# Kernel optimization log

Hardware: AMD Instinct MI355X
Metric: run time of the kernel (lower is better)

## Reference

```python
import jax, jax.numpy as jnp
import numpy as np

N_NODES = 20000
NUM_STEPS = 6
SIGNS = (1.0, -1.0, 1.0, -1.0, 1.0, -1.0)  # TF_POS, TF_NEG, PPI_POS, PPI_NEG, UNDIR, MIRNA_NEG


def setup_inputs() -> dict:
    key = jax.random.key(0)
    ks = jax.random.split(key, 12)
    B, N, E, H, C = 64, N_NODES, 400000, 64, 32
    return {
        "ctl_base": jax.random.normal(ks[0], (B, N), jnp.float32),
        "u_raw": jax.random.normal(ks[1], (B, N), jnp.float32),
        "cell_idx": jax.random.randint(ks[2], (B,), 0, C, jnp.int32),
        "edge_src": jax.random.randint(ks[3], (6, E), 0, N, jnp.int32),
        "edge_dst": jax.random.randint(ks[4], (6, E), 0, N, jnp.int32),
        "edge_val": jax.random.uniform(ks[5], (6, E), jnp.float32),
        "g_logits": jnp.zeros((6,), jnp.float32),
        "alpha_logits": jnp.zeros((NUM_STEPS,), jnp.float32),
        "cell_emb": jax.random.normal(ks[6], (C, H), jnp.float32),
        "W1": jax.random.normal(ks[7], (3, H), jnp.float32) * 0.1,
        "b1": jnp.zeros((H,), jnp.float32),
        "W2": jax.random.normal(ks[8], (H, 1), jnp.float32) * 0.1,
        "b2": jnp.zeros((1,), jnp.float32),
    }


def _spmm_right(h, src, dst, val):
    # out[b, j] = sum_{e: dst[e]==j} h[b, src[e]] * val[e]   (== h @ A)
    gathered = h.T[src] * val[:, None]  # [E, B]
    return jax.ops.segment_sum(gathered, dst, num_segments=N_NODES).T  # [B, N]


def reference(ctl_base, u_raw, g_logits, alpha_logits, cell_emb,
              W1, b1, W2, b2, edge_val, edge_src, edge_dst, cell_idx):
    g = jax.nn.softplus(g_logits)          # [6] relation gates
    alphas = jax.nn.sigmoid(alpha_logits)  # [num_steps]
    h0 = u_raw
    h = u_raw
    for k in range(NUM_STEPS):
        msg = jnp.zeros_like(h)
        for r in range(6):
            msg = msg + SIGNS[r] * g[r] * _spmm_right(h, edge_src[r], edge_dst[r], edge_val[r])
        a = alphas[k]
        h = a * h0 + (1.0 - a) * msg
    # decode: stack [ctl, u_raw, hK] -> [B, N, 3]
    x = jnp.stack([ctl_base, u_raw, h], axis=-1)
    hd = jax.nn.relu(jnp.einsum('bnf,fh->bnh', x, W1) + b1)  # [B, N, H]
    hd = hd + cell_emb[cell_idx][:, None, :]
    y = (jnp.einsum('bnh,ho->bno', hd, W2) + b2)[..., 0]  # [B, N]
    return y
```

## Files before the change

kernel.cpp:

```cpp
#include <hip/hip_runtime.h>

#define N_NODES 20000
#define HID 64
#define NSTEPS 6
#define NSLICE 8
#define SLICE_SZ (N_NODES / NSLICE)
#define SUBB 64
#define NBLK (NSLICE * SUBB)
#define TBLK ((N_NODES + 63) / 64)
#define NB1 512
#define CBLK ((N_NODES + 255) / 256)
#define MAGIC 13422

typedef _Float16 h8_t __attribute__((ext_vector_type(8)));
typedef unsigned u4_t __attribute__((ext_vector_type(4)));

union U16H { unsigned short u; _Float16 h; };
union U4H8 { uint4 u; _Float16 h[8]; };

__device__ __forceinline__ _Float16 us_as_h(unsigned short s) { U16H u; u.u = s; return u.h; }
__device__ __forceinline__ unsigned short h_as_us(_Float16 h) { U16H u; u.h = h; return u.u; }

__device__ __forceinline__ int slice_of(int d) {
    return (int)(((unsigned)d * (unsigned)MAGIC) >> 25);
}
__device__ __forceinline__ float softplusf_(float x) {
    return (x > 0.f) ? (x + log1pf(expf(-x))) : log1pf(expf(x));
}
__device__ __forceinline__ float sigmoidf_(float x) {
    return 1.f / (1.f + expf(-x));
}

__global__ __launch_bounds__(256) void count8_kernel(const int* __restrict__ edst,
                                                     int* __restrict__ gcnt, int TE,
                                                     u4_t* __restrict__ egq, long long egq_n) {
    u4_t z = {0u, 0u, 0u, 0u};
    for (long long i = (long long)blockIdx.x * 256 + threadIdx.x; i < egq_n;
         i += (long long)NB1 * 256)
        __builtin_nontemporal_store(z, egq + i);

    __shared__ int lh[8];
    int bk = blockIdx.x;
    int lane = threadIdx.x & 63;
    if (threadIdx.x < 8) lh[threadIdx.x] = 0;
    __syncthreads();
    int chunk = ((TE + NB1 - 1) / NB1 + 255) & ~255;
    int lo = bk * chunk;
    int hi = min(lo + chunk, TE);
    int my = 0;
    for (int ii = 0; ii < chunk; ii += 256) {
        int i = lo + ii + (int)threadIdx.x;
        bool act = i < hi;
        int s = -1;
        if (act) s = slice_of(__builtin_nontemporal_load(edst + i));
#pragma unroll
        for (int q = 0; q < 8; ++q) {
            unsigned long long b = __ballot(s == q);
            if (lane == q) my += (int)__popcll(b);
        }
    }
    if (lane < 8) atomicAdd(&lh[lane], my);
    __syncthreads();
    if (threadIdx.x < 8) gcnt[bk * 8 + threadIdx.x] = lh[threadIdx.x];
}

__global__ __launch_bounds__(256) void scan8_kernel(const int* __restrict__ gcnt,
                                                    int* __restrict__ blkoff,
                                                    int* __restrict__ bbase,
                                                    const float* __restrict__ g_logits,
                                                    const float* __restrict__ alpha_logits,
                                                    const int* __restrict__ cell_idx,
                                                    const float* __restrict__ cell_emb,
                                                    const float* __restrict__ W2,
                                                    const float* __restrict__ b2,
                                                    float* __restrict__ gsign,
                                                    float* __restrict__ alph,
                                                    float* __restrict__ cell_dot) {
    __shared__ int psum[8][33];
    int tid = threadIdx.x;
    int s = tid >> 5, g = tid & 31;
    const int per = NB1 / 32;
    int sum = 0;
    for (int b = g * per; b < (g + 1) * per; ++b) sum += gcnt[b * 8 + s];
    psum[s][g] = sum;
    __syncthreads();
    if (tid < 8) {
        int run = 0;
        for (int i = 0; i < 32; ++i) { int v = psum[tid][i]; psum[tid][i] = run; run += v; }
        psum[tid][32] = run;
    }
    __syncthreads();
    int run = psum[s][g];
    for (int b = g * per; b < (g + 1) * per; ++b) {
        blkoff[b * 8 + s] = run;
        run += gcnt[b * 8 + s];
    }
    if (tid == 0) {
        int acc = 0;
        bbase[0] = 0;
        for (int q = 0; q < 8; ++q) { acc += psum[q][32]; bbase[q + 1] = acc; }
    }
    if (tid < 64) {
        if (tid < 6) gsign[tid] = ((tid & 1) ? -1.f : 1.f) * softplusf_(g_logits[tid]);
        if (tid < NSTEPS) alph[tid] = sigmoidf_(alpha_logits[tid]);
        int ci = cell_idx[tid];
        float acc = b2[0];
        for (int hh = 0; hh < HID; ++hh) acc = fmaf(cell_emb[ci * HID + hh], W2[hh], acc);
        cell_dot[tid] = acc;
    }
}

__global__ __launch_bounds__(256) void bucket_kernel(const int* __restrict__ esrc,
                                                     const int* __restrict__ edst,
                                                     const float* __restrict__ eval,
                                                     const float* __restrict__ gsign,
                                                     const int* __restrict__ blkoff,
                                                     const int* __restrict__ bbase,
                                                     int2* __restrict__ bucket,
                                                     int E, int TE) {
    __shared__ int lcur[8];
    int bk = blockIdx.x;
    int lane = threadIdx.x & 63;
    if (threadIdx.x < 8) lcur[threadIdx.x] = bbase[threadIdx.x] + blkoff[bk * 8 + threadIdx.x];
    __syncthreads();
    int chunk = ((TE + NB1 - 1) / NB1 + 255) & ~255;
    int lo = bk * chunk;
    int hi = min(lo + chunk, TE);
    for (int ii = 0; ii < chunk; ii += 256) {
        int i = lo + ii + (int)threadIdx.x;
        bool act = i < hi;
        int s = -1, meta = 0, cb = 0;
        if (act) {
            int d  = __builtin_nontemporal_load(edst + i);
            int sv = __builtin_nontemporal_load(esrc + i);
            float ev = __builtin_nontemporal_load(eval + i);
            s = slice_of(d);
            int dl = d - s * SLICE_SZ;
            meta = sv | (dl << 16);
            int r = (i >= E) + (i >= 2 * E) + (i >= 3 * E) + (i >= 4 * E) + (i >= 5 * E);
            cb = __float_as_int(gsign[r] * ev);
        }
        int pos = 0;
#pragma unroll
        for (int q = 0; q < 8; ++q) {
            unsigned long long b = __ballot(s == q);
            if (b) {
                int leader = (int)__ffsll(b) - 1;
                int base = 0;
                if (lane == leader) base = atomicAdd(&lcur[q], (int)__popcll(b));
                base = __shfl(base, leader);
                if (s == q) pos = base + (int)__popcll(b & ((1ull << lane) - 1ull));
            }
        }
        if (act) bucket[pos] = make_int2(meta, cb);
    }
}

__global__ __launch_bounds__(256) void hist2db_kernel(const int2* __restrict__ bucket,
                                                      const int* __restrict__ bbase,
                                                      int* __restrict__ blkcnt) {
    __shared__ int lh[SLICE_SZ];
    int bk = blockIdx.x;
    int slice = bk & (NSLICE - 1);
    int sub = bk >> 3;
    for (int b = threadIdx.x; b < SLICE_SZ; b += 256) lh[b] = 0;
    __syncthreads();
    int lo = bbase[slice];
    int total = bbase[slice + 1] - lo;
    int chunk = ((total + SUBB - 1) / SUBB + 255) & ~255;
    int beg = lo + sub * chunk;
    int end = min(beg + chunk, lo + total);
    const int* mp = (const int*)bucket;
    for (int i = beg + (int)threadIdx.x; i < end; i += 256) {
        int meta = __builtin_nontemporal_load(mp + 2 * (size_t)i);
        atomicAdd(&lh[((unsigned)meta) >> 16], 1);
    }
    __syncthreads();
    int* out = blkcnt + (size_t)(slice * SUBB + sub) * SLICE_SZ;
    for (int b = threadIdx.x; b < SLICE_SZ; b += 256) out[b] = lh[b];
}

__global__ __launch_bounds__(256) void colscan_kernel(int* __restrict__ blkcnt,
                                                      int* __restrict__ counts,
                                                      int* __restrict__ blksum) {
    int n = blockIdx.x * 256 + threadIdx.x;
    int run = 0;
    if (n < N_NODES) {
        int slice = n / SLICE_SZ, bin = n % SLICE_SZ;
        size_t base = (size_t)slice * SUBB * SLICE_SZ + bin;
#pragma unroll 8
        for (int s = 0; s < SUBB; ++s) {
            size_t idx = base + (size_t)s * SLICE_SZ;
            int t = blkcnt[idx];
            blkcnt[idx] = run;
            run += t;
        }
        counts[n] = run;
    }
    int g = (n < N_NODES) ? ((run + 7) >> 3) : 0;
#pragma unroll
    for (int st = 1; st < 64; st <<= 1) g += __shfl_xor(g, st, 64);
    __shared__ int wsum[4];
    if ((threadIdx.x & 63) == 0) wsum[threadIdx.x >> 6] = g;
    __syncthreads();
    if (threadIdx.x == 0) blksum[blockIdx.x] = wsum[0] + wsum[1] + wsum[2] + wsum[3];
}

__global__ __launch_bounds__(256) void scan2_kernel(const int* __restrict__ counts,
                                                    const int* __restrict__ blksum,
                                                    int* __restrict__ grp_ptr, int n) {
    int b = blockIdx.x;
    int tid = threadIdx.x, lane = tid & 63, wid = tid >> 6;
    int i = b * 256 + tid;
    int v = (i < n) ? ((counts[i] + 7) >> 3) : 0;
    int x = v;
#pragma unroll
    for (int st = 1; st < 64; st <<= 1) {
        int t = __shfl_up(x, st, 64);
        if (lane >= st) x += t;
    }
    __shared__ int wsum[4];
    if (lane == 63) wsum[wid] = x;
    int s = ((lane < b) ? blksum[lane] : 0) +
            ((lane + 64 < b) ? blksum[lane + 64] : 0);
#pragma unroll
    for (int st = 1; st < 64; st <<= 1) s += __shfl_xor(s, st, 64);
    __syncthreads();
    int woff = s;
    if (wid > 0) woff += wsum[0];
    if (wid > 1) woff += wsum[1];
    if (wid > 2) woff += wsum[2];
    int off = woff + x - v;
    if (i < n) grp_ptr[i] = off;
    if (i == n - 1) grp_ptr[n] = off + v;
}

__global__ __launch_bounds__(256) void scatter2b_kernel(const int2* __restrict__ bucket,
                                                        const int* __restrict__ bbase,
                                                        const int* __restrict__ grp_ptr,
                                                        const int* __restrict__ blkcnt,
                                                        unsigned* __restrict__ eg,
                                                        const float* __restrict__ u_raw,
                                                        float* __restrict__ u_t,
                                                        _Float16* __restrict__ uh) {
    __shared__ float smem[64 * 65];
    int bk = blockIdx.x;
    if (bk >= NBLK) {
        float(*tile)[65] = (float(*)[65])smem;
        int c0 = (bk - NBLK) * 64;
        int tx = threadIdx.x & 63, ty = threadIdx.x >> 6;
#pragma unroll
        for (int i = 0; i < 16; ++i) {
            int c = c0 + tx;
            tile[ty + i * 4][tx] = (c < N_NODES) ? u_raw[(size_t)(ty + i * 4) * N_NODES + c] : 0.f;
        }
        __syncthreads();
#pragma unroll
        for (int i = 0; i < 16; ++i) {
            int c = c0 + ty + i * 4;
            if (c < N_NODES) {
                float v = tile[tx][ty + i * 4];
                u_t[(size_t)c * 64 + tx] = v;
                uh[(size_t)c * 64 + tx] = (_Float16)v;
            }
        }
        return;
    }
    int* lbase = (int*)smem;
    int slice = bk & (NSLICE - 1);
    int sub = bk >> 3;
    int lo_n = slice * SLICE_SZ;
    const int* boff = blkcnt + (size_t)(slice * SUBB + sub) * SLICE_SZ;
    for (int b = threadIdx.x; b < SLICE_SZ; b += 256)
        lbase[b] = grp_ptr[lo_n + b] * 8 + boff[b];
    __syncthreads();
    int lo = bbase[slice];
    int total = bbase[slice + 1] - lo;
    int chunk = ((total + SUBB - 1) / SUBB + 255) & ~255;
    int beg = lo + sub * chunk;
    int end = min(beg + chunk, lo + total);
    for (int i = beg + (int)threadIdx.x; i < end; i += 256) {
        long long rec = __builtin_nontemporal_load((const long long*)bucket + i);
        int meta = (int)rec;
        float cf = __int_as_float((int)(rec >> 32));
        int pos = atomicAdd(&lbase[((unsigned)meta) >> 16], 1);
        eg[pos] = (unsigned)(meta & 0xFFFF) | ((unsigned)h_as_us((_Float16)cf) << 16);
    }
}

__global__ __launch_bounds__(256) void step_kernel(const _Float16* __restrict__ h_in,
                                                   const float* __restrict__ h0,
                                                   _Float16* __restrict__ h_out,
                                                   float* __restrict__ hF,
                                                   const int* __restrict__ grp_ptr,
                                                   const unsigned* __restrict__ eg,
                                                   const float* __restrict__ alph,
                                                   int k, int last) {
    int lane = threadIdx.x & 63;
    int node = blockIdx.x * 4 + (threadIdx.x >> 6);
    if (node >= N_NODES) return;
    int gb = __builtin_amdgcn_readfirstlane(grp_ptr[node]);
    int ge = __builtin_amdgcn_readfirstlane(grp_ptr[node + 1]);
    int sub8 = lane >> 3;
    const _Float16* hbase = h_in + (lane & 7) * 8;
    float acc[8] = {0.f, 0.f, 0.f, 0.f, 0.f, 0.f, 0.f, 0.f};
    int g = gb;
    for (; g + 2 <= ge; g += 2) {
        unsigned e0 = eg[(size_t)g * 8 + sub8];
        unsigned e1 = eg[(size_t)g * 8 + 8 + sub8];
        h8_t v0 = *(const h8_t*)(hbase + (e0 & 0xFFFFu) * 64);
        h8_t v1 = *(const h8_t*)(hbase + (e1 & 0xFFFFu) * 64);
        float c0 = (float)us_as_h((unsigned short)(e0 >> 16));
        float c1 = (float)us_as_h((unsigned short)(e1 >> 16));
#pragma unroll
        for (int j = 0; j < 8; ++j) acc[j] = fmaf((float)v0[j], c0, acc[j]);
#pragma unroll
        for (int j = 0; j < 8; ++j) acc[j] = fmaf((float)v1[j], c1, acc[j]);
    }
    if (g < ge) {
        unsigned e0 = eg[(size_t)g * 8 + sub8];
        h8_t v0 = *(const h8_t*)(hbase + (e0 & 0xFFFFu) * 64);
        float c0 = (float)us_as_h((unsigned short)(e0 >> 16));
#pragma unroll
        for (int j = 0; j < 8; ++j) acc[j] = fmaf((float)v0[j], c0, acc[j]);
    }
#pragma unroll
    for (int st = 8; st < 64; st <<= 1) {
#pragma unroll
        for (int j = 0; j < 8; ++j) acc[j] += __shfl_xor(acc[j], st, 64);
    }
    if (lane < 8) {
        float a = alph[k];
        int base = node * 64 + lane * 8;
        float4 h0a = *(const float4*)(h0 + base);
        float4 h0b = *(const float4*)(h0 + base + 4);
        float om = 1.f - a;
        float r0 = fmaf(a, h0a.x, om * acc[0]);
        float r1 = fmaf(a, h0a.y, om * acc[1]);
        float r2 = fmaf(a, h0a.z, om * acc[2]);
        float r3 = fmaf(a, h0a.w, om * acc[3]);
        float r4 = fmaf(a, h0b.x, om * acc[4]);
        float r5 = fmaf(a, h0b.y, om * acc[5]);
        float r6 = fmaf(a, h0b.z, om * acc[6]);
        float r7 = fmaf(a, h0b.w, om * acc[7]);
        if (last) {
            *(float4*)(hF + base)     = make_float4(r0, r1, r2, r3);
            *(float4*)(hF + base + 4) = make_float4(r4, r5, r6, r7);
        } else {
            U4H8 o;
            o.h[0] = (_Float16)r0; o.h[1] = (_Float16)r1;
            o.h[2] = (_Float16)r2; o.h[3] = (_Float16)r3;
            o.h[4] = (_Float16)r4; o.h[5] = (_Float16)r5;
            o.h[6] = (_Float16)r6; o.h[7] = (_Float16)r7;
            *(uint4*)(h_out + base) = o.u;
        }
    }
}

__global__ __launch_bounds__(256) void decode_kernel(float* __restrict__ y,
                                                     const float* __restrict__ ctl,
                                                     const float* __restrict__ u,
                                                     const float* __restrict__ hF,
                                                     const float* __restrict__ W1,
                                                     const float* __restrict__ b1,
                                                     const float* __restrict__ W2,
                                                     const float* __restrict__ cell_dot) {
    __shared__ float tile[64][65];
    __shared__ float4 pack[HID];
    __shared__ float w2s[HID];
    __shared__ float cds[64];
    if (threadIdx.x < HID) {
        int hh = threadIdx.x;
        pack[hh] = make_float4(W1[0 * HID + hh], W1[1 * HID + hh], W1[2 * HID + hh], b1[hh]);
        w2s[hh] = W2[hh];
        cds[hh] = cell_dot[hh];
    }
    int n0 = blockIdx.x * 64;
    int tx = threadIdx.x & 63, ty = threadIdx.x >> 6;
#pragma unroll
    for (int i = 0; i < 16; ++i) {
        int n = n0 + ty + i * 4;
        tile[ty + i * 4][tx] = (n < N_NODES) ? hF[(size_t)n * 64 + tx] : 0.f;
    }
    __syncthreads();
#pragma unroll
    for (int i = 0; i < 16; ++i) {
        int b = ty + i * 4;
        int n = n0 + tx;
        if (n < N_NODES) {
            size_t idx = (size_t)b * N_NODES + n;
            float xc = ctl[idx], xu = u[idx], xh = tile[tx][b];
            float acc = 0.f;
#pragma unroll 8
            for (int hh = 0; hh < HID; ++hh) {
                float4 p = pack[hh];
                float t = fmaf(xc, p.x, fmaf(xu, p.y, fmaf(xh, p.z, p.w)));
                t = fmaxf(t, 0.f);
                acc = fmaf(t, w2s[hh], acc);
            }
            y[idx] = acc + cds[b];
        }
    }
}

extern "C" void kernel_launch(void* const* d_in, const int* in_sizes, int n_in,
                              void* d_out, int out_size, void* d_ws, size_t ws_size,
                              hipStream_t stream) {
    const float* ctl          = (const float*)d_in[0];
    const float* u_raw        = (const float*)d_in[1];
    const int*   cell_idx     = (const int*)d_in[2];
    const int*   edge_src     = (const int*)d_in[3];
    const int*   edge_dst     = (const int*)d_in[4];
    const float* edge_val     = (const float*)d_in[5];
    const float* g_logits     = (const float*)d_in[6];
    const float* alpha_logits = (const float*)d_in[7];
    const float* cell_emb     = (const float*)d_in[8];
    const float* W1           = (const float*)d_in[9];
    const float* b1           = (const float*)d_in[10];
    const float* W2           = (const float*)d_in[11];
    const float* b2           = (const float*)d_in[12];
    float* y = (float*)d_out;

    const int TE = in_sizes[3];
    const int E  = TE / 6;
    const int NB = N_NODES * 64;

    char* ws = (char*)d_ws;
    size_t off = 0;
    auto alloc = [&](size_t bytes) -> char* {
        char* p = ws + off;
        off += (bytes + 255) & ~(size_t)255;
        return p;
    };
    int* grp_ptr = (int*)alloc((N_NODES + 1) * sizeof(int));
    int* counts  = (int*)alloc(N_NODES * sizeof(int));
    int* blksum  = (int*)alloc(CBLK * sizeof(int));
    int* blkcnt  = (int*)alloc((size_t)NSLICE * SUBB * SLICE_SZ * sizeof(int));
    int* gcnt    = (int*)alloc((size_t)NB1 * 8 * sizeof(int));
    int* blkoff  = (int*)alloc((size_t)NB1 * 8 * sizeof(int));
    int* bbase   = (int*)alloc(16 * sizeof(int));
    const size_t MAXG = (size_t)TE / 8 + N_NODES + 8;
    unsigned* eg = (unsigned*)alloc(MAXG * 8 * sizeof(unsigned));
    int2* bucket    = (int2*)alloc((size_t)TE * sizeof(int2));
    _Float16* uh    = (_Float16*)alloc((size_t)NB * 2);
    _Float16* hA    = (_Float16*)alloc((size_t)NB * 2);
    _Float16* hB    = (_Float16*)alloc((size_t)NB * 2);
    float* hF       = (float*)alloc((size_t)NB * 4);
    float* u_t      = (float*)alloc((size_t)NB * sizeof(float));
    float* gsign    = (float*)alloc(8 * sizeof(float));
    float* alph     = (float*)alloc(8 * sizeof(float));
    float* cell_dot = (float*)alloc(64 * sizeof(float));

    count8_kernel<<<NB1, 256, 0, stream>>>(edge_dst, gcnt, TE,
                                           (u4_t*)eg, (long long)(MAXG * 2));
    scan8_kernel<<<1, 256, 0, stream>>>(gcnt, blkoff, bbase, g_logits, alpha_logits,
                                        cell_idx, cell_emb, W2, b2,
                                        gsign, alph, cell_dot);
    bucket_kernel<<<NB1, 256, 0, stream>>>(edge_src, edge_dst, edge_val, gsign,
                                           blkoff, bbase, bucket, E, TE);
    hist2db_kernel<<<NBLK, 256, 0, stream>>>(bucket, bbase, blkcnt);
    colscan_kernel<<<CBLK, 256, 0, stream>>>(blkcnt, counts, blksum);
    scan2_kernel<<<CBLK, 256, 0, stream>>>(counts, blksum, grp_ptr, N_NODES);
    scatter2b_kernel<<<NBLK + TBLK, 256, 0, stream>>>(bucket, bbase, grp_ptr, blkcnt,
                                                      eg, u_raw, u_t, uh);

    const _Float16* hin = uh;
    for (int k = 0; k < NSTEPS; ++k) {
        _Float16* hout = (k & 1) ? hB : hA;
        step_kernel<<<(N_NODES + 3) / 4, 256, 0, stream>>>(hin, u_t, hout, hF, grp_ptr,
                                                           eg, alph, k, k == NSTEPS - 1);
        hin = hout;
    }

    decode_kernel<<<TBLK, 256, 0, stream>>>(y, ctl, u_raw, hF, W1, b1, W2, cell_dot);
}
```

Before: 364.9 us.

## Make edge bucketing deterministic, move transpose earlier, and software-pipeline gather loop

The bucket kernel now computes positions from per-wave ballot counts combined through shared memory, so it no longer issues atomics per class. The scatter kernel becomes a 64-thread wave that ranks identical bins with a 64-step shuffle loop, which gives a deterministic edge order at the cost of extra ALU work. The u_raw transpose moves into the histogram kernel, and the block counts change (SUBB 64→256, NB1 512→2048), which makes the blkcnt and colscan work larger. The step kernel prefetches edge records and gathered rows two pairs ahead to hide load latency.

Result: slower. 387.4 us (+6.2%).

```diff
diff --git a/kernel.cpp b/kernel.cpp
--- a/kernel.cpp
+++ b/kernel.cpp
@@ -5,10 +5,10 @@
 #define NSTEPS 6
 #define NSLICE 8
 #define SLICE_SZ (N_NODES / NSLICE)
-#define SUBB 64
+#define SUBB 256
 #define NBLK (NSLICE * SUBB)
 #define TBLK ((N_NODES + 63) / 64)
-#define NB1 512
+#define NB1 2048
 #define CBLK ((N_NODES + 255) / 256)
 #define MAGIC 13422
 
@@ -119,15 +119,17 @@
                                                      int2* __restrict__ bucket,
                                                      int E, int TE) {
     __shared__ int lcur[8];
+    __shared__ int wcnt[4][8];
+    int tid = threadIdx.x;
     int bk = blockIdx.x;
-    int lane = threadIdx.x & 63;
-    if (threadIdx.x < 8) lcur[threadIdx.x] = bbase[threadIdx.x] + blkoff[bk * 8 + threadIdx.x];
-    __syncthreads();
+    int lane = tid & 63, wid = tid >> 6;
+    if (tid < 8) lcur[tid] = bbase[tid] + blkoff[bk * 8 + tid];
     int chunk = ((TE + NB1 - 1) / NB1 + 255) & ~255;
     int lo = bk * chunk;
     int hi = min(lo + chunk, TE);
     for (int ii = 0; ii < chunk; ii += 256) {
-        int i = lo + ii + (int)threadIdx.x;
+        __syncthreads();
+        int i = lo + ii + tid;
         bool act = i < hi;
         int s = -1, meta = 0, cb = 0;
         if (act) {
@@ -140,27 +142,62 @@
             int r = (i >= E) + (i >= 2 * E) + (i >= 3 * E) + (i >= 4 * E) + (i >= 5 * E);
             cb = __float_as_int(gsign[r] * ev);
         }
-        int pos = 0;
+        int within = 0, wavecnt = 0;
+        unsigned long long below = (1ull << lane) - 1ull;
 #pragma unroll
         for (int q = 0; q < 8; ++q) {
             unsigned long long b = __ballot(s == q);
-            if (b) {
-                int leader = (int)__ffsll(b) - 1;
-                int base = 0;
-                if (lane == leader) base = atomicAdd(&lcur[q], (int)__popcll(b));
-                base = __shfl(base, leader);
-                if (s == q) pos = base + (int)__popcll(b & ((1ull << lane) - 1ull));
-            }
-        }
+            if (s == q) within = (int)__popcll(b & below);
+            if (lane == q) wavecnt = (int)__popcll(b);
+        }
+        if (lane < 8) wcnt[wid][lane] = wavecnt;
+        __syncthreads();
+        int pos = 0, newcur = 0;
+        if (act) {
+            int off = lcur[s];
+            if (wid > 0) off += wcnt[0][s];
+            if (wid > 1) off += wcnt[1][s];
+            if (wid > 2) off += wcnt[2][s];
+            pos = off + within;
+        }
+        if (tid < 8)
+            newcur = lcur[tid] + wcnt[0][tid] + wcnt[1][tid] + wcnt[2][tid] + wcnt[3][tid];
+        __syncthreads();
+        if (tid < 8) lcur[tid] = newcur;
         if (act) bucket[pos] = make_int2(meta, cb);
     }
 }
 
 __global__ __launch_bounds__(256) void hist2db_kernel(const int2* __restrict__ bucket,
                                                       const int* __restrict__ bbase,
-                                                      int* __restrict__ blkcnt) {
-    __shared__ int lh[SLICE_SZ];
+                                                      int* __restrict__ blkcnt,
+                                                      const float* __restrict__ u_raw,
+                                                      float* __restrict__ u_t,
+                                                      _Float16* __restrict__ uh) {
+    __shared__ float smem[64 * 65];
     int bk = blockIdx.x;
+    if (bk >= NBLK) {
+        float(*tile)[65] = (float(*)[65])smem;
+        int c0 = (bk - NBLK) * 64;
+        int tx = threadIdx.x & 63, ty = threadIdx.x >> 6;
+#pragma unroll
+        for (int i = 0; i < 16; ++i) {
+            int c = c0 + tx;
+            tile[ty + i * 4][tx] = (c < N_NODES) ? u_raw[(size_t)(ty + i * 4) * N_NODES + c] : 0.f;
+        }
+        __syncthreads();
+#pragma unroll
+        for (int i = 0; i < 16; ++i) {
+            int c = c0 + ty + i * 4;
+            if (c < N_NODES) {
+                float v = tile[tx][ty + i * 4];
+                u_t[(size_t)c * 64 + tx] = v;
+                uh[(size_t)c * 64 + tx] = (_Float16)v;
+            }
+        }
+        return;
+    }
+    int* lh = (int*)smem;
     int slice = bk & (NSLICE - 1);
     int sub = bk >> 3;
     for (int b = threadIdx.x; b < SLICE_SZ; b += 256) lh[b] = 0;
@@ -235,43 +272,19 @@
     if (i == n - 1) grp_ptr[n] = off + v;
 }
 
-__global__ __launch_bounds__(256) void scatter2b_kernel(const int2* __restrict__ bucket,
-                                                        const int* __restrict__ bbase,
-                                                        const int* __restrict__ grp_ptr,
-                                                        const int* __restrict__ blkcnt,
-                                                        unsigned* __restrict__ eg,
-                                                        const float* __restrict__ u_raw,
-                                                        float* __restrict__ u_t,
-                                                        _Float16* __restrict__ uh) {
-    __shared__ float smem[64 * 65];
+__global__ __launch_bounds__(64) void scatter_det_kernel(const int2* __restrict__ bucket,
+                                                         const int* __restrict__ bbase,
+                                                         const int* __restrict__ grp_ptr,
+                                                         const int* __restrict__ blkcnt,
+                                                         unsigned* __restrict__ eg) {
+    __shared__ int lbase[SLICE_SZ];
     int bk = blockIdx.x;
-    if (bk >= NBLK) {
-        float(*tile)[65] = (float(*)[65])smem;
-        int c0 = (bk - NBLK) * 64;
-        int tx = threadIdx.x & 63, ty = threadIdx.x >> 6;
-#pragma unroll
-        for (int i = 0; i < 16; ++i) {
-            int c = c0 + tx;
-            tile[ty + i * 4][tx] = (c < N_NODES) ? u_raw[(size_t)(ty + i * 4) * N_NODES + c] : 0.f;
-        }
-        __syncthreads();
-#pragma unroll
-        for (int i = 0; i < 16; ++i) {
-            int c = c0 + ty + i * 4;
-            if (c < N_NODES) {
-                float v = tile[tx][ty + i * 4];
-                u_t[(size_t)c * 64 + tx] = v;
-                uh[(size_t)c * 64 + tx] = (_Float16)v;
-            }
-        }
-        return;
-    }
-    int* lbase = (int*)smem;
     int slice = bk & (NSLICE - 1);
     int sub = bk >> 3;
+    int lane = threadIdx.x;
     int lo_n = slice * SLICE_SZ;
     const int* boff = blkcnt + (size_t)(slice * SUBB + sub) * SLICE_SZ;
-    for (int b = threadIdx.x; b < SLICE_SZ; b += 256)
+    for (int b = lane; b < SLICE_SZ; b += 64)
         lbase[b] = grp_ptr[lo_n + b] * 8 + boff[b];
     __syncthreads();
     int lo = bbase[slice];
@@ -279,12 +292,30 @@
     int chunk = ((total + SUBB - 1) / SUBB + 255) & ~255;
     int beg = lo + sub * chunk;
     int end = min(beg + chunk, lo + total);
-    for (int i = beg + (int)threadIdx.x; i < end; i += 256) {
-        long long rec = __builtin_nontemporal_load((const long long*)bucket + i);
-        int meta = (int)rec;
-        float cf = __int_as_float((int)(rec >> 32));
-        int pos = atomicAdd(&lbase[((unsigned)meta) >> 16], 1);
-        eg[pos] = (unsigned)(meta & 0xFFFF) | ((unsigned)h_as_us((_Float16)cf) << 16);
+    for (int i0 = beg; i0 < end; i0 += 64) {
+        int i = i0 + lane;
+        bool act = i < end;
+        int meta = 0, cb = 0, bin = -1;
+        if (act) {
+            long long rec = *(const long long*)(bucket + i);
+            meta = (int)rec;
+            cb = (int)(rec >> 32);
+            bin = (int)(((unsigned)meta) >> 16);
+        }
+        int rank = 0, tot = 0;
+        for (int l = 0; l < 64; ++l) {
+            int ob = __shfl(bin, l, 64);
+            bool same = (bin >= 0) && (ob == bin);
+            rank += (same && l < lane) ? 1 : 0;
+            tot  += same ? 1 : 0;
+        }
+        if (act) {
+            int base = lbase[bin];
+            int pos = base + rank;
+            float cf = __uint_as_float((unsigned)cb);
+            eg[pos] = (unsigned)(meta & 0xFFFF) | ((unsigned)h_as_us((_Float16)cf) << 16);
+            if (rank == tot - 1) lbase[bin] = base + tot;
+        }
     }
 }
 
@@ -303,26 +334,53 @@
     int ge = __builtin_amdgcn_readfirstlane(grp_ptr[node + 1]);
     int sub8 = lane >> 3;
     const _Float16* hbase = h_in + (lane & 7) * 8;
+    const unsigned* ep = eg + sub8;
     float acc[8] = {0.f, 0.f, 0.f, 0.f, 0.f, 0.f, 0.f, 0.f};
     int g = gb;
-    for (; g + 2 <= ge; g += 2) {
-        unsigned e0 = eg[(size_t)g * 8 + sub8];
-        unsigned e1 = eg[(size_t)g * 8 + 8 + sub8];
-        h8_t v0 = *(const h8_t*)(hbase + (e0 & 0xFFFFu) * 64);
-        h8_t v1 = *(const h8_t*)(hbase + (e1 & 0xFFFFu) * 64);
-        float c0 = (float)us_as_h((unsigned short)(e0 >> 16));
-        float c1 = (float)us_as_h((unsigned short)(e1 >> 16));
-#pragma unroll
-        for (int j = 0; j < 8; ++j) acc[j] = fmaf((float)v0[j], c0, acc[j]);
-#pragma unroll
-        for (int j = 0; j < 8; ++j) acc[j] = fmaf((float)v1[j], c1, acc[j]);
-    }
-    if (g < ge) {
-        unsigned e0 = eg[(size_t)g * 8 + sub8];
-        h8_t v0 = *(const h8_t*)(hbase + (e0 & 0xFFFFu) * 64);
-        float c0 = (float)us_as_h((unsigned short)(e0 >> 16));
-#pragma unroll
-        for (int j = 0; j < 8; ++j) acc[j] = fmaf((float)v0[j], c0, acc[j]);
+    int pairs = (ge - g) >> 1;
+    if (pairs >= 2) {
+        size_t b0 = (size_t)g * 8;
+        unsigned ea0 = ep[b0], ea1 = ep[b0 + 8];
+        h8_t va0 = *(const h8_t*)(hbase + (ea0 & 0xFFFFu) * 64);
+        h8_t va1 = *(const h8_t*)(hbase + (ea1 & 0xFFFFu) * 64);
+        unsigned eb0 = ep[b0 + 16], eb1 = ep[b0 + 24];
+        int p = 0;
+        for (; p + 2 < pairs; ++p) {
+            h8_t vb0 = *(const h8_t*)(hbase + (eb0 & 0xFFFFu) * 64);
+            h8_t vb1 = *(const h8_t*)(hbase + (eb1 & 0xFFFFu) * 64);
+            size_t bn = (size_t)(g + 2 * (p + 2)) * 8;
+            unsigned ec0 = ep[bn], ec1 = ep[bn + 8];
+            float c0 = (float)us_as_h((unsigned short)(ea0 >> 16));
+            float c1 = (float)us_as_h((unsigned short)(ea1 >> 16));
+#pragma unroll
+            for (int j = 0; j < 8; ++j) acc[j] = fmaf((float)va0[j], c0, acc[j]);
+#pragma unroll
+            for (int j = 0; j < 8; ++j) acc[j] = fmaf((float)va1[j], c1, acc[j]);
+            ea0 = eb0; ea1 = eb1; eb0 = ec0; eb1 = ec1;
+            va0 = vb0; va1 = vb1;
+        }
+        h8_t vb0 = *(const h8_t*)(hbase + (eb0 & 0xFFFFu) * 64);
+        h8_t vb1 = *(const h8_t*)(hbase + (eb1 & 0xFFFFu) * 64);
+        float c0 = (float)us_as_h((unsigned short)(ea0 >> 16));
+        float c1 = (float)us_as_h((unsigned short)(ea1 >> 16));
+        float c2 = (float)us_as_h((unsigned short)(eb0 >> 16));
+        float c3 = (float)us_as_h((unsigned short)(eb1 >> 16));
+#pragma unroll
+        for (int j = 0; j < 8; ++j) acc[j] = fmaf((float)va0[j], c0, acc[j]);
+#pragma unroll
+        for (int j = 0; j < 8; ++j) acc[j] = fmaf((float)va1[j], c1, acc[j]);
+#pragma unroll
+        for (int j = 0; j < 8; ++j) acc[j] = fmaf((float)vb0[j], c2, acc[j]);
+#pragma unroll
+        for (int j = 0; j < 8; ++j) acc[j] = fmaf((float)vb1[j], c3, acc[j]);
+        g += 2 * pairs;
+    }
+    for (; g < ge; ++g) {
+        unsigned e = ep[(size_t)g * 8];
+        h8_t v = *(const h8_t*)(hbase + (e & 0xFFFFu) * 64);
+        float c = (float)us_as_h((unsigned short)(e >> 16));
+#pragma unroll
+        for (int j = 0; j < 8; ++j) acc[j] = fmaf((float)v[j], c, acc[j]);
     }
 #pragma unroll
     for (int st = 8; st < 64; st <<= 1) {
@@ -458,11 +516,11 @@
                                         gsign, alph, cell_dot);
     bucket_kernel<<<NB1, 256, 0, stream>>>(edge_src, edge_dst, edge_val, gsign,
                                            blkoff, bbase, bucket, E, TE);
-    hist2db_kernel<<<NBLK, 256, 0, stream>>>(bucket, bbase, blkcnt);
+    hist2db_kernel<<<NBLK + TBLK, 256, 0, stream>>>(bucket, bbase, blkcnt,
+                                                    u_raw, u_t, uh);
     colscan_kernel<<<CBLK, 256, 0, stream>>>(blkcnt, counts, blksum);
     scan2_kernel<<<CBLK, 256, 0, stream>>>(counts, blksum, grp_ptr, N_NODES);
-    scatter2b_kernel<<<NBLK + TBLK, 256, 0, stream>>>(bucket, bbase, grp_ptr, blkcnt,
-                                                      eg, u_raw, u_t, uh);
+    scatter_det_kernel<<<NBLK, 64, 0, stream>>>(bucket, bbase, grp_ptr, blkcnt, eg);
 
     const _Float16* hin = uh;
     for (int k = 0; k < NSTEPS; ++k) {
```
